# Optimization experiments

Measured on AMD Instinct MI355X. Metric: run time of the kernel, lower is better.

Reference implementation:

```python
import jax, jax.numpy as jnp
import numpy as np

B, L, D_PAIR, N_HEAD = 1, 320, 128, 4
EPS = 1e-5


def setup_inputs() -> dict:
    key = jax.random.key(0)
    ks = jax.random.split(key, 8)
    s = 0.05  # ~xavier scale for fan_in=128
    return {
        "pair": jax.random.normal(ks[0], (B, L, L, D_PAIR), jnp.float32),
        "norm_w": jnp.ones((D_PAIR,), jnp.float32),
        "norm_b": jnp.zeros((D_PAIR,), jnp.float32),
        "Wq": jax.random.normal(ks[1], (D_PAIR, D_PAIR), jnp.float32) * s,
        "Wk": jax.random.normal(ks[2], (D_PAIR, D_PAIR), jnp.float32) * s,
        "Wv": jax.random.normal(ks[3], (D_PAIR, D_PAIR), jnp.float32) * s,
        "Wg": jax.random.normal(ks[4], (D_PAIR, D_PAIR), jnp.float32) * s,
        "bg": jnp.zeros((D_PAIR,), jnp.float32),
        "Wo": jax.random.normal(ks[5], (D_PAIR, D_PAIR), jnp.float32) * s,
        "bo": jnp.zeros((D_PAIR,), jnp.float32),
        "Wb": jax.random.normal(ks[6], (N_HEAD, D_PAIR), jnp.float32) * s,
    }


def reference(pair, norm_w, norm_b, Wq, Wk, Wv, Wg, bg, Wo, bo, Wb):
    # Triangle attention, mode='start' (no permute). pair: (B, L, L, D)
    Bs, Ls, _, D = pair.shape
    H = Wb.shape[0]
    Dh = D // H
    scale = Dh ** -0.5

    # LayerNorm (fp32, matches torch eps=1e-5)
    mu = jnp.mean(pair, axis=-1, keepdims=True)
    var = jnp.var(pair, axis=-1, keepdims=True)
    x = (pair - mu) * jax.lax.rsqrt(var + EPS) * norm_w + norm_b

    def heads(y):
        # (B,L,L,D) -> (B,L,H,L,Dh): attention runs along the second L axis per row i
        return y.reshape(Bs, Ls, Ls, H, Dh).transpose(0, 1, 3, 2, 4)

    Q = heads(x @ Wq.T)
    K = heads(x @ Wk.T)
    V = heads(x @ Wv.T)
    g = heads(jax.nn.sigmoid(x @ Wg.T + bg))

    attn = jnp.einsum('blhid,blhjd->blhij', Q, K) * scale  # (B,L,H,L,L)
    # bias from RAW pair (pre-norm), projected to heads, broadcast over query index i
    bias = (pair @ Wb.T).transpose(0, 1, 3, 2)[:, :, :, None, :]  # (B,L,H,1,L)
    attn = jax.nn.softmax(attn + bias, axis=-1)

    out = jnp.einsum('blhij,blhjd->blhid', attn, V)  # (B,L,H,L,Dh)
    out = (g * out).transpose(0, 1, 3, 2, 4).reshape(Bs, Ls, Ls, D)
    return pair + out @ Wo.T + bo
```

## Files before the change

### kernel.cpp

```cpp
#include <hip/hip_runtime.h>

typedef unsigned short u16;
typedef unsigned int u32;
typedef __attribute__((ext_vector_type(8))) short bf16x8;
typedef __attribute__((ext_vector_type(4))) float f32x4;
typedef __attribute__((ext_vector_type(2))) unsigned int u32x2;

#define LOG2E 1.4426950408889634f

__device__ __forceinline__ u16 f2bf(float f) {
    u32 u = __float_as_uint(f);
    u += 0x7fffu + ((u >> 16) & 1u);
    return (u16)(u >> 16);
}
__device__ __forceinline__ float bf2f(u16 s) {
    return __uint_as_float(((u32)s) << 16);
}
__device__ __forceinline__ u32 pk_bf_trunc(float hi, float lo) {
    return __builtin_amdgcn_perm(__float_as_uint(hi), __float_as_uint(lo), 0x07060302u);
}

__global__ void wconv_kernel(const float* __restrict__ Wq, const float* __restrict__ Wk,
                             const float* __restrict__ Wv, const float* __restrict__ Wg,
                             const float* __restrict__ Wo, u16* __restrict__ wbf) {
    int idx = blockIdx.x * blockDim.x + threadIdx.x;
    wbf[0 * 16384 + idx] = f2bf(Wq[idx]);
    wbf[1 * 16384 + idx] = f2bf(Wk[idx]);
    wbf[2 * 16384 + idx] = f2bf(Wv[idx]);
    wbf[3 * 16384 + idx] = f2bf(Wg[idx]);
    wbf[4 * 16384 + idx] = f2bf(Wo[idx]);
}

#define PBUF_W 2688
#define QS_OFF 21504
#define KS_OFF 34304
#define GS_OFF 47104
#define VTS_OFF 59904

__global__ __launch_bounds__(512, 2)
void attn_kernel(const float* __restrict__ pair,
                 const float* __restrict__ norm_w,
                 const float* __restrict__ norm_b,
                 const float* __restrict__ bg,
                 const float* __restrict__ Wb,
                 const u16* __restrict__ wbf,
                 u16* __restrict__ Obf) {
    const int l = blockIdx.x >> 2;
    const int h = blockIdx.x & 3;
    const int tid = threadIdx.x;
    const int wave = tid >> 6;
    const int lane = tid & 63;
    const int i_lo = lane & 15;
    const int q = lane >> 4;

    __shared__ __align__(16) u16 smem[70400];
    __shared__ __align__(16) float biasLds[320];
    __shared__ __align__(16) float wls[3 * 128];

    if (tid < 96) {
        int a = tid >> 5;
        int t = tid & 31;
        const float* src = (a == 0) ? norm_w : (a == 1) ? norm_b : (Wb + h * 128);
        f32x4 v = *(const f32x4*)(src + t * 4);
        *(f32x4*)&wls[a * 128 + t * 4] = v;
    }

    float bg0 = bg[h * 32 + i_lo];
    float bg1 = bg[h * 32 + 16 + i_lo];

    bf16x8 wfrag[4][8];
#pragma unroll
    for (int kc = 0; kc < 4; ++kc)
#pragma unroll
        for (int nt = 0; nt < 8; ++nt) {
            int mat = nt >> 1;
            int drow = h * 32 + (nt & 1) * 16 + i_lo;
            wfrag[kc][nt] = *(const bf16x8*)&wbf[mat * 16384 + drow * 128 + kc * 32 + q * 8];
        }

    __syncthreads();

    const int row_g = tid >> 2;
    const int c4 = tid & 3;

#pragma unroll 1
    for (int t = 0; t < 3; ++t) {
        const int j0 = t * 128;
        const int nrows = (t == 2) ? 64 : 128;
        const bool act = row_g < nrows;

        f32x4 pr[8];
        float mu, rs, bd;
        if (act) {
            const float* prow = pair + ((size_t)(l * 320 + j0 + row_g)) * 128 + c4 * 32;
#pragma unroll
            for (int u = 0; u < 8; ++u) pr[u] = *(const f32x4*)(prow + u * 4);
            float s = 0.f, s2 = 0.f;
            bd = 0.f;
#pragma unroll
            for (int u = 0; u < 8; ++u) {
                f32x4 p = pr[u];
                f32x4 wb4 = *(const f32x4*)&wls[2 * 128 + c4 * 32 + u * 4];
                s += p[0] + p[1] + p[2] + p[3];
                s2 += p[0] * p[0] + p[1] * p[1] + p[2] * p[2] + p[3] * p[3];
                bd += p[0] * wb4[0] + p[1] * wb4[1] + p[2] * wb4[2] + p[3] * wb4[3];
            }
            s += __shfl_xor(s, 1);   s += __shfl_xor(s, 2);
            s2 += __shfl_xor(s2, 1); s2 += __shfl_xor(s2, 2);
            bd += __shfl_xor(bd, 1); bd += __shfl_xor(bd, 2);
            mu = s * 0.0078125f;
            float var = s2 * 0.0078125f - mu * mu;
            rs = rsqrtf(var + 1e-5f);
        }

        __syncthreads();
        if (act) {
#pragma unroll
            for (int u = 0; u < 8; ++u) {
                f32x4 p = pr[u];
                f32x4 w4 = *(const f32x4*)&wls[0 * 128 + c4 * 32 + u * 4];
                f32x4 b4 = *(const f32x4*)&wls[1 * 128 + c4 * 32 + u * 4];
                ushort4 xv;
                xv.x = f2bf((p[0] - mu) * rs * w4[0] + b4[0]);
                xv.y = f2bf((p[1] - mu) * rs * w4[1] + b4[1]);
                xv.z = f2bf((p[2] - mu) * rs * w4[2] + b4[2]);
                xv.w = f2bf((p[3] - mu) * rs * w4[3] + b4[3]);
                *(ushort4*)&smem[row_g * 136 + c4 * 32 + u * 4] = xv;
            }
            if (c4 == 0) biasLds[j0 + row_g] = bd * LOG2E;
        }
        __syncthreads();

        if (wave * 16 < nrows) {
            f32x4 acc[8];
#pragma unroll
            for (int nt = 0; nt < 8; ++nt) acc[nt] = (f32x4){0.f, 0.f, 0.f, 0.f};
#pragma unroll
            for (int kc = 0; kc < 4; ++kc) {
                bf16x8 a = *(const bf16x8*)&smem[(wave * 16 + i_lo) * 136 + kc * 32 + q * 8];
#pragma unroll
                for (int nt = 0; nt < 8; ++nt)
                    acc[nt] = __builtin_amdgcn_mfma_f32_16x16x32_bf16(a, wfrag[kc][nt], acc[nt], 0, 0, 0);
            }
            int jrow = j0 + wave * 16 + q * 4;
#pragma unroll
            for (int nt = 0; nt < 8; ++nt) {
#pragma unroll
                for (int r = 0; r < 4; ++r) {
                    float v = acc[nt][r];
                    int jr = jrow + r;
                    int dl = (nt & 1) * 16 + i_lo;
                    if (nt < 2)      smem[QS_OFF + jr * 40 + dl] = f2bf(v);
                    else if (nt < 4) smem[KS_OFF + jr * 40 + dl] = f2bf(v);
                    else if (nt < 6) smem[VTS_OFF + dl * 328 + jr] = f2bf(v);
                    else {
                        float z = v + ((nt & 1) ? bg1 : bg0);
                        float g = 1.0f / (1.0f + exp2f(-z * LOG2E));
                        smem[GS_OFF + jr * 40 + dl] = f2bf(g);
                    }
                }
            }
        }
    }
    __syncthreads();

    const float SC = 0.17677669529663687f * LOG2E;
    const f32x4 zero4 = {0.f, 0.f, 0.f, 0.f};
    u16* pb = smem + wave * PBUF_W;
#pragma unroll 1
    for (int t2 = 0; t2 < 3; ++t2) {
        const int strip = wave + 8 * t2;
        if (strip >= 20) break;
        const int i0 = strip * 16;
        bf16x8 qf = *(const bf16x8*)&smem[QS_OFF + (i0 + i_lo) * 40 + q * 8];

        f32x4 sc[20];
#pragma unroll
        for (int jt = 0; jt < 20; ++jt) {
            bf16x8 kf = *(const bf16x8*)&smem[KS_OFF + (jt * 16 + i_lo) * 40 + q * 8];
            sc[jt] = __builtin_amdgcn_mfma_f32_16x16x32_bf16(kf, qf, zero4, 0, 0, 0);
        }
        float sum = 0.f;
#pragma unroll
        for (int jt = 0; jt < 20; ++jt) {
            f32x4 b4 = *(const f32x4*)&biasLds[jt * 16 + q * 4];
#pragma unroll
            for (int r = 0; r < 4; ++r) {
                float p = exp2f(sc[jt][r] * SC + b4[r]);
                sc[jt][r] = p;
                sum += p;
            }
        }
        sum += __shfl_xor(sum, 16);
        sum += __shfl_xor(sum, 32);
        float rinv = 1.0f / sum;

        f32x4 oacc[2];
        oacc[0] = zero4; oacc[1] = zero4;
#pragma unroll
        for (int hh = 0; hh < 2; ++hh) {
#pragma unroll
            for (int jt10 = 0; jt10 < 10; ++jt10) {
                f32x4 s4 = sc[hh * 10 + jt10];
                u32x2 pk;
                pk.x = pk_bf_trunc(s4[1], s4[0]);
                pk.y = pk_bf_trunc(s4[3], s4[2]);
                *(u32x2*)&pb[i_lo * 168 + jt10 * 16 + q * 4] = pk;
            }
#pragma unroll
            for (int kt = 0; kt < 5; ++kt) {
                bf16x8 pf = *(const bf16x8*)&pb[i_lo * 168 + kt * 32 + q * 8];
#pragma unroll
                for (int mt = 0; mt < 2; ++mt) {
                    bf16x8 vf = *(const bf16x8*)&smem[VTS_OFF + (mt * 16 + i_lo) * 328 + hh * 160 + kt * 32 + q * 8];
                    oacc[mt] = __builtin_amdgcn_mfma_f32_16x16x32_bf16(vf, pf, oacc[mt], 0, 0, 0);
                }
            }
        }
#pragma unroll
        for (int mt = 0; mt < 2; ++mt) {
            ushort4 g4 = *(const ushort4*)&smem[GS_OFF + (i0 + i_lo) * 40 + mt * 16 + q * 4];
            float o0 = oacc[mt][0] * rinv * bf2f(g4.x);
            float o1 = oacc[mt][1] * rinv * bf2f(g4.y);
            float o2 = oacc[mt][2] * rinv * bf2f(g4.z);
            float o3 = oacc[mt][3] * rinv * bf2f(g4.w);
            u32x2 pk;
            pk.x = pk_bf_trunc(o1, o0);
            pk.y = pk_bf_trunc(o3, o2);
            *(u32x2*)&Obf[((size_t)(l * 320 + i0 + i_lo)) * 128 + h * 32 + mt * 16 + q * 4] = pk;
        }
    }
}

__global__ __launch_bounds__(256)
void outproj_kernel(const float* __restrict__ pair,
                    const float* __restrict__ bo,
                    const u16* __restrict__ Obf,
                    const u16* __restrict__ wbf,
                    float* __restrict__ out) {
    const int tid = threadIdx.x;
    const int wave = tid >> 6;
    const int lane = tid & 63;
    const int i_lo = lane & 15;
    const int q = lane >> 4;
    const int mrow = blockIdx.x * 64 + wave * 16;
    const u16* Wo = wbf + 4 * 16384;

    bf16x8 of[4];
#pragma unroll
    for (int kc = 0; kc < 4; ++kc)
        of[kc] = *(const bf16x8*)&Obf[((size_t)(mrow + i_lo)) * 128 + kc * 32 + q * 8];

    f32x4 acc[8];
#pragma unroll
    for (int nt = 0; nt < 8; ++nt) acc[nt] = (f32x4){0.f, 0.f, 0.f, 0.f};
#pragma unroll
    for (int nt = 0; nt < 8; ++nt) {
#pragma unroll
        for (int kc = 0; kc < 4; ++kc) {
            bf16x8 wf = *(const bf16x8*)&Wo[(nt * 16 + i_lo) * 128 + kc * 32 + q * 8];
            acc[nt] = __builtin_amdgcn_mfma_f32_16x16x32_bf16(wf, of[kc], acc[nt], 0, 0, 0);
        }
    }
#pragma unroll
    for (int nt = 0; nt < 8; ++nt) {
        size_t idx = ((size_t)(mrow + i_lo)) * 128 + nt * 16 + q * 4;
        f32x4 p4 = *(const f32x4*)&pair[idx];
        f32x4 b4 = *(const f32x4*)&bo[nt * 16 + q * 4];
        f32x4 o4;
        o4[0] = acc[nt][0] + p4[0] + b4[0];
        o4[1] = acc[nt][1] + p4[1] + b4[1];
        o4[2] = acc[nt][2] + p4[2] + b4[2];
        o4[3] = acc[nt][3] + p4[3] + b4[3];
        *(f32x4*)&out[idx] = o4;
    }
}

extern "C" void kernel_launch(void* const* d_in, const int* in_sizes, int n_in,
                              void* d_out, int out_size, void* d_ws, size_t ws_size,
                              hipStream_t stream) {
    const float* pair   = (const float*)d_in[0];
    const float* norm_w = (const float*)d_in[1];
    const float* norm_b = (const float*)d_in[2];
    const float* Wq     = (const float*)d_in[3];
    const float* Wk     = (const float*)d_in[4];
    const float* Wv     = (const float*)d_in[5];
    const float* Wg     = (const float*)d_in[6];
    const float* bg     = (const float*)d_in[7];
    const float* Wo     = (const float*)d_in[8];
    const float* bo     = (const float*)d_in[9];
    const float* Wb     = (const float*)d_in[10];

    u16* wbf = (u16*)d_ws;
    u16* Obf = wbf + 5 * 16384;
    float* out = (float*)d_out;

    wconv_kernel<<<64, 256, 0, stream>>>(Wq, Wk, Wv, Wg, Wo, wbf);
    attn_kernel<<<320 * 4, 512, 0, stream>>>(pair, norm_w, norm_b, bg, Wb, wbf, Obf);
    outproj_kernel<<<1600, 256, 0, stream>>>(pair, bo, Obf, wbf, out);
}
```

Measured before the change: 291.0 us.

## Shrink attention LDS and registers to raise occupancy; move gating into outproj

Cuts shared memory from about 140KB to about 65KB and raises launch bounds to 4 blocks per CU. To get there, Q is kept in registers instead of LDS, the gate is written to a global buffer and applied in the output-projection kernel, and projection weights are loaded from global memory per tile instead of held in registers. The projection now runs over 64-row tiles, with the Q/K and V/G column halves split across wave groups. Softmax and PV are processed in 64-column chunks so fewer score registers are live. The trade-off is extra global traffic for the gate buffer, repeated weight loads and more barriers, plus a second bf16 rounding of the gated output.

```diff
diff --git a/kernel.cpp b/kernel.cpp
--- a/kernel.cpp
+++ b/kernel.cpp
@@ -31,20 +31,19 @@
     wbf[4 * 16384 + idx] = f2bf(Wo[idx]);
 }
 
-#define PBUF_W 2688
-#define QS_OFF 21504
-#define KS_OFF 34304
-#define GS_OFF 47104
-#define VTS_OFF 59904
-
-__global__ __launch_bounds__(512, 2)
+#define KS_OFF 9216
+#define VTS_OFF 22016
+#define PB_W 1152
+
+__global__ __launch_bounds__(512, 4)
 void attn_kernel(const float* __restrict__ pair,
                  const float* __restrict__ norm_w,
                  const float* __restrict__ norm_b,
                  const float* __restrict__ bg,
                  const float* __restrict__ Wb,
                  const u16* __restrict__ wbf,
-                 u16* __restrict__ Obf) {
+                 u16* __restrict__ Obf,
+                 u16* __restrict__ Gg) {
     const int l = blockIdx.x >> 2;
     const int h = blockIdx.x & 3;
     const int tid = threadIdx.x;
@@ -53,9 +52,9 @@
     const int i_lo = lane & 15;
     const int q = lane >> 4;
 
-    __shared__ __align__(16) u16 smem[70400];
+    __shared__ __align__(16) u16 smem[32512];
     __shared__ __align__(16) float biasLds[320];
-    __shared__ __align__(16) float wls[3 * 128];
+    __shared__ __align__(16) float wls[384];
 
     if (tid < 96) {
         int a = tid >> 5;
@@ -68,165 +67,166 @@
     float bg0 = bg[h * 32 + i_lo];
     float bg1 = bg[h * 32 + 16 + i_lo];
 
-    bf16x8 wfrag[4][8];
-#pragma unroll
-    for (int kc = 0; kc < 4; ++kc)
-#pragma unroll
-        for (int nt = 0; nt < 8; ++nt) {
-            int mat = nt >> 1;
-            int drow = h * 32 + (nt & 1) * 16 + i_lo;
-            wfrag[kc][nt] = *(const bf16x8*)&wbf[mat * 16384 + drow * 128 + kc * 32 + q * 8];
-        }
-
     __syncthreads();
 
-    const int row_g = tid >> 2;
-    const int c4 = tid & 3;
+    const int row_g = tid >> 3;
+    const int c8 = tid & 7;
+    const int wrow = (wave & 3) * 16;
+    const int nth_flip = wave >> 2;
+
+    u32 qkeep[3][4];
 
 #pragma unroll 1
-    for (int t = 0; t < 3; ++t) {
-        const int j0 = t * 128;
-        const int nrows = (t == 2) ? 64 : 128;
-        const bool act = row_g < nrows;
-
-        f32x4 pr[8];
-        float mu, rs, bd;
-        if (act) {
-            const float* prow = pair + ((size_t)(l * 320 + j0 + row_g)) * 128 + c4 * 32;
-#pragma unroll
-            for (int u = 0; u < 8; ++u) pr[u] = *(const f32x4*)(prow + u * 4);
-            float s = 0.f, s2 = 0.f;
-            bd = 0.f;
-#pragma unroll
-            for (int u = 0; u < 8; ++u) {
-                f32x4 p = pr[u];
-                f32x4 wb4 = *(const f32x4*)&wls[2 * 128 + c4 * 32 + u * 4];
-                s += p[0] + p[1] + p[2] + p[3];
-                s2 += p[0] * p[0] + p[1] * p[1] + p[2] * p[2] + p[3] * p[3];
-                bd += p[0] * wb4[0] + p[1] * wb4[1] + p[2] * wb4[2] + p[3] * wb4[3];
-            }
-            s += __shfl_xor(s, 1);   s += __shfl_xor(s, 2);
-            s2 += __shfl_xor(s2, 1); s2 += __shfl_xor(s2, 2);
-            bd += __shfl_xor(bd, 1); bd += __shfl_xor(bd, 2);
-            mu = s * 0.0078125f;
-            float var = s2 * 0.0078125f - mu * mu;
-            rs = rsqrtf(var + 1e-5f);
-        }
+    for (int t = 0; t < 5; ++t) {
+        const int j0 = t * 64;
+        const float* prow = pair + ((size_t)(l * 320 + j0 + row_g)) * 128 + c8 * 16;
+        f32x4 pr[4];
+#pragma unroll
+        for (int u = 0; u < 4; ++u) pr[u] = *(const f32x4*)(prow + u * 4);
+
+        float s = 0.f, s2 = 0.f, bd = 0.f;
+#pragma unroll
+        for (int u = 0; u < 4; ++u) {
+            f32x4 p = pr[u];
+            f32x4 wb4 = *(const f32x4*)&wls[256 + c8 * 16 + u * 4];
+            s += p[0] + p[1] + p[2] + p[3];
+            s2 += p[0] * p[0] + p[1] * p[1] + p[2] * p[2] + p[3] * p[3];
+            bd += p[0] * wb4[0] + p[1] * wb4[1] + p[2] * wb4[2] + p[3] * wb4[3];
+        }
+        s += __shfl_xor(s, 1);   s += __shfl_xor(s, 2);   s += __shfl_xor(s, 4);
+        s2 += __shfl_xor(s2, 1); s2 += __shfl_xor(s2, 2); s2 += __shfl_xor(s2, 4);
+        bd += __shfl_xor(bd, 1); bd += __shfl_xor(bd, 2); bd += __shfl_xor(bd, 4);
+        float mu = s * 0.0078125f;
+        float var = s2 * 0.0078125f - mu * mu;
+        float rs = rsqrtf(var + 1e-5f);
 
         __syncthreads();
-        if (act) {
-#pragma unroll
-            for (int u = 0; u < 8; ++u) {
-                f32x4 p = pr[u];
-                f32x4 w4 = *(const f32x4*)&wls[0 * 128 + c4 * 32 + u * 4];
-                f32x4 b4 = *(const f32x4*)&wls[1 * 128 + c4 * 32 + u * 4];
-                ushort4 xv;
-                xv.x = f2bf((p[0] - mu) * rs * w4[0] + b4[0]);
-                xv.y = f2bf((p[1] - mu) * rs * w4[1] + b4[1]);
-                xv.z = f2bf((p[2] - mu) * rs * w4[2] + b4[2]);
-                xv.w = f2bf((p[3] - mu) * rs * w4[3] + b4[3]);
-                *(ushort4*)&smem[row_g * 136 + c4 * 32 + u * 4] = xv;
-            }
-            if (c4 == 0) biasLds[j0 + row_g] = bd * LOG2E;
-        }
+#pragma unroll
+        for (int u = 0; u < 4; ++u) {
+            f32x4 p = pr[u];
+            f32x4 w4 = *(const f32x4*)&wls[0 + c8 * 16 + u * 4];
+            f32x4 b4 = *(const f32x4*)&wls[128 + c8 * 16 + u * 4];
+            ushort4 xv;
+            xv.x = f2bf((p[0] - mu) * rs * w4[0] + b4[0]);
+            xv.y = f2bf((p[1] - mu) * rs * w4[1] + b4[1]);
+            xv.z = f2bf((p[2] - mu) * rs * w4[2] + b4[2]);
+            xv.w = f2bf((p[3] - mu) * rs * w4[3] + b4[3]);
+            *(ushort4*)&smem[row_g * 136 + c8 * 16 + u * 4] = xv;
+        }
+        if (c8 == 0) biasLds[j0 + row_g] = bd * LOG2E;
         __syncthreads();
 
-        if (wave * 16 < nrows) {
-            f32x4 acc[8];
-#pragma unroll
-            for (int nt = 0; nt < 8; ++nt) acc[nt] = (f32x4){0.f, 0.f, 0.f, 0.f};
-#pragma unroll
-            for (int kc = 0; kc < 4; ++kc) {
-                bf16x8 a = *(const bf16x8*)&smem[(wave * 16 + i_lo) * 136 + kc * 32 + q * 8];
-#pragma unroll
-                for (int nt = 0; nt < 8; ++nt)
-                    acc[nt] = __builtin_amdgcn_mfma_f32_16x16x32_bf16(a, wfrag[kc][nt], acc[nt], 0, 0, 0);
-            }
-            int jrow = j0 + wave * 16 + q * 4;
-#pragma unroll
-            for (int nt = 0; nt < 8; ++nt) {
+        const int nth = (t & 1) ^ nth_flip;
+        f32x4 acc[4];
+#pragma unroll
+        for (int n2 = 0; n2 < 4; ++n2) acc[n2] = (f32x4){0.f, 0.f, 0.f, 0.f};
+#pragma unroll
+        for (int kc = 0; kc < 4; ++kc) {
+            bf16x8 a = *(const bf16x8*)&smem[(wrow + i_lo) * 136 + kc * 32 + q * 8];
+#pragma unroll
+            for (int n2 = 0; n2 < 4; ++n2) {
+                int nt = nth * 4 + n2;
+                bf16x8 wf = *(const bf16x8*)&wbf[(nt >> 1) * 16384 +
+                                                 (h * 32 + (nt & 1) * 16 + i_lo) * 128 + kc * 32 + q * 8];
+                acc[n2] = __builtin_amdgcn_mfma_f32_16x16x32_bf16(a, wf, acc[n2], 0, 0, 0);
+            }
+        }
+        const int jrow = j0 + wrow + q * 4;
+        if (nth == 0) {
+            const int ti = t >> 1;
+#pragma unroll
+            for (int dd = 0; dd < 2; ++dd)
+#pragma unroll
+                for (int rr = 0; rr < 2; ++rr)
+                    qkeep[ti][dd * 2 + rr] =
+                        (u32)f2bf(acc[dd][rr * 2]) | ((u32)f2bf(acc[dd][rr * 2 + 1]) << 16);
+#pragma unroll
+            for (int n2 = 2; n2 < 4; ++n2)
+#pragma unroll
+                for (int r = 0; r < 4; ++r)
+                    smem[KS_OFF + (jrow + r) * 40 + (n2 & 1) * 16 + i_lo] = f2bf(acc[n2][r]);
+        } else {
+#pragma unroll
+            for (int n2 = 0; n2 < 2; ++n2)
+#pragma unroll
+                for (int r = 0; r < 4; ++r)
+                    smem[VTS_OFF + (n2 * 16 + i_lo) * 328 + jrow + r] = f2bf(acc[n2][r]);
+#pragma unroll
+            for (int n2 = 2; n2 < 4; ++n2)
 #pragma unroll
                 for (int r = 0; r < 4; ++r) {
-                    float v = acc[nt][r];
-                    int jr = jrow + r;
-                    int dl = (nt & 1) * 16 + i_lo;
-                    if (nt < 2)      smem[QS_OFF + jr * 40 + dl] = f2bf(v);
-                    else if (nt < 4) smem[KS_OFF + jr * 40 + dl] = f2bf(v);
-                    else if (nt < 6) smem[VTS_OFF + dl * 328 + jr] = f2bf(v);
-                    else {
-                        float z = v + ((nt & 1) ? bg1 : bg0);
-                        float g = 1.0f / (1.0f + exp2f(-z * LOG2E));
-                        smem[GS_OFF + jr * 40 + dl] = f2bf(g);
-                    }
+                    float z = acc[n2][r] + ((n2 & 1) ? bg1 : bg0);
+                    float g = 1.0f / (1.0f + exp2f(-z * LOG2E));
+                    Gg[((size_t)((l * 4 + h) * 320 + jrow + r)) * 32 + (n2 & 1) * 16 + i_lo] = f2bf(g);
                 }
-            }
         }
     }
     __syncthreads();
 
     const float SC = 0.17677669529663687f * LOG2E;
     const f32x4 zero4 = {0.f, 0.f, 0.f, 0.f};
-    u16* pb = smem + wave * PBUF_W;
+    u16* pb = smem + wave * PB_W;
+    const int nstrip = (wave < 4) ? 3 : 2;
 #pragma unroll 1
-    for (int t2 = 0; t2 < 3; ++t2) {
-        const int strip = wave + 8 * t2;
-        if (strip >= 20) break;
-        const int i0 = strip * 16;
-        bf16x8 qf = *(const bf16x8*)&smem[QS_OFF + (i0 + i_lo) * 40 + q * 8];
-
-        f32x4 sc[20];
-#pragma unroll
-        for (int jt = 0; jt < 20; ++jt) {
-            bf16x8 kf = *(const bf16x8*)&smem[KS_OFF + (jt * 16 + i_lo) * 40 + q * 8];
-            sc[jt] = __builtin_amdgcn_mfma_f32_16x16x32_bf16(kf, qf, zero4, 0, 0, 0);
-        }
+    for (int t2 = 0; t2 < nstrip; ++t2) {
+        const int i0 = (wave + 8 * t2) * 16;
+#pragma unroll
+        for (int dd = 0; dd < 2; ++dd)
+#pragma unroll
+            for (int rr = 0; rr < 2; ++rr) {
+                u32 v = qkeep[t2][dd * 2 + rr];
+                pb[(q * 4 + rr * 2) * 40 + dd * 16 + i_lo] = (u16)v;
+                pb[(q * 4 + rr * 2 + 1) * 40 + dd * 16 + i_lo] = (u16)(v >> 16);
+            }
+        bf16x8 qf = *(const bf16x8*)&pb[i_lo * 40 + q * 8];
+
+        f32x4 oacc[2];
+        oacc[0] = zero4; oacc[1] = zero4;
         float sum = 0.f;
-#pragma unroll
-        for (int jt = 0; jt < 20; ++jt) {
-            f32x4 b4 = *(const f32x4*)&biasLds[jt * 16 + q * 4];
-#pragma unroll
-            for (int r = 0; r < 4; ++r) {
-                float p = exp2f(sc[jt][r] * SC + b4[r]);
-                sc[jt][r] = p;
-                sum += p;
+#pragma unroll 1
+        for (int c = 0; c < 5; ++c) {
+            f32x4 sc4[4];
+#pragma unroll
+            for (int jt = 0; jt < 4; ++jt) {
+                bf16x8 kf = *(const bf16x8*)&smem[KS_OFF + (c * 64 + jt * 16 + i_lo) * 40 + q * 8];
+                sc4[jt] = __builtin_amdgcn_mfma_f32_16x16x32_bf16(kf, qf, zero4, 0, 0, 0);
+            }
+#pragma unroll
+            for (int jt = 0; jt < 4; ++jt) {
+                f32x4 b4 = *(const f32x4*)&biasLds[c * 64 + jt * 16 + q * 4];
+#pragma unroll
+                for (int r = 0; r < 4; ++r) {
+                    float p = exp2f(sc4[jt][r] * SC + b4[r]);
+                    sc4[jt][r] = p;
+                    sum += p;
+                }
+            }
+#pragma unroll
+            for (int jt = 0; jt < 4; ++jt) {
+                u32x2 pk;
+                pk.x = pk_bf_trunc(sc4[jt][1], sc4[jt][0]);
+                pk.y = pk_bf_trunc(sc4[jt][3], sc4[jt][2]);
+                *(u32x2*)&pb[i_lo * 72 + jt * 16 + q * 4] = pk;
+            }
+#pragma unroll
+            for (int kt2 = 0; kt2 < 2; ++kt2) {
+                bf16x8 pf = *(const bf16x8*)&pb[i_lo * 72 + kt2 * 32 + q * 8];
+#pragma unroll
+                for (int mt = 0; mt < 2; ++mt) {
+                    bf16x8 vf = *(const bf16x8*)&smem[VTS_OFF + (mt * 16 + i_lo) * 328 +
+                                                      c * 64 + kt2 * 32 + q * 8];
+                    oacc[mt] = __builtin_amdgcn_mfma_f32_16x16x32_bf16(vf, pf, oacc[mt], 0, 0, 0);
+                }
             }
         }
         sum += __shfl_xor(sum, 16);
         sum += __shfl_xor(sum, 32);
         float rinv = 1.0f / sum;
-
-        f32x4 oacc[2];
-        oacc[0] = zero4; oacc[1] = zero4;
-#pragma unroll
-        for (int hh = 0; hh < 2; ++hh) {
-#pragma unroll
-            for (int jt10 = 0; jt10 < 10; ++jt10) {
-                f32x4 s4 = sc[hh * 10 + jt10];
-                u32x2 pk;
-                pk.x = pk_bf_trunc(s4[1], s4[0]);
-                pk.y = pk_bf_trunc(s4[3], s4[2]);
-                *(u32x2*)&pb[i_lo * 168 + jt10 * 16 + q * 4] = pk;
-            }
-#pragma unroll
-            for (int kt = 0; kt < 5; ++kt) {
-                bf16x8 pf = *(const bf16x8*)&pb[i_lo * 168 + kt * 32 + q * 8];
-#pragma unroll
-                for (int mt = 0; mt < 2; ++mt) {
-                    bf16x8 vf = *(const bf16x8*)&smem[VTS_OFF + (mt * 16 + i_lo) * 328 + hh * 160 + kt * 32 + q * 8];
-                    oacc[mt] = __builtin_amdgcn_mfma_f32_16x16x32_bf16(vf, pf, oacc[mt], 0, 0, 0);
-                }
-            }
-        }
 #pragma unroll
         for (int mt = 0; mt < 2; ++mt) {
-            ushort4 g4 = *(const ushort4*)&smem[GS_OFF + (i0 + i_lo) * 40 + mt * 16 + q * 4];
-            float o0 = oacc[mt][0] * rinv * bf2f(g4.x);
-            float o1 = oacc[mt][1] * rinv * bf2f(g4.y);
-            float o2 = oacc[mt][2] * rinv * bf2f(g4.z);
-            float o3 = oacc[mt][3] * rinv * bf2f(g4.w);
             u32x2 pk;
-            pk.x = pk_bf_trunc(o1, o0);
-            pk.y = pk_bf_trunc(o3, o2);
+            pk.x = pk_bf_trunc(oacc[mt][1] * rinv, oacc[mt][0] * rinv);
+            pk.y = pk_bf_trunc(oacc[mt][3] * rinv, oacc[mt][2] * rinv);
             *(u32x2*)&Obf[((size_t)(l * 320 + i0 + i_lo)) * 128 + h * 32 + mt * 16 + q * 4] = pk;
         }
     }
@@ -236,6 +236,7 @@
 void outproj_kernel(const float* __restrict__ pair,
                     const float* __restrict__ bo,
                     const u16* __restrict__ Obf,
+                    const u16* __restrict__ Gg,
                     const u16* __restrict__ wbf,
                     float* __restrict__ out) {
     const int tid = threadIdx.x;
@@ -243,13 +244,26 @@
     const int lane = tid & 63;
     const int i_lo = lane & 15;
     const int q = lane >> 4;
-    const int mrow = blockIdx.x * 64 + wave * 16;
+    const int blk = blockIdx.x;
+    const int mrow = blk * 64 + wave * 16;
+    const int lidx = blk / 5;
+    const int irow = mrow - lidx * 320 + i_lo;
     const u16* Wo = wbf + 4 * 16384;
 
     bf16x8 of[4];
 #pragma unroll
-    for (int kc = 0; kc < 4; ++kc)
-        of[kc] = *(const bf16x8*)&Obf[((size_t)(mrow + i_lo)) * 128 + kc * 32 + q * 8];
+    for (int kc = 0; kc < 4; ++kc) {
+        union { bf16x8 v; u32 u[4]; } A, G, R;
+        A.v = *(const bf16x8*)&Obf[((size_t)(mrow + i_lo)) * 128 + kc * 32 + q * 8];
+        G.v = *(const bf16x8*)&Gg[((size_t)((lidx * 4 + kc) * 320 + irow)) * 32 + q * 8];
+#pragma unroll
+        for (int k4 = 0; k4 < 4; ++k4) {
+            float lo = __uint_as_float(A.u[k4] << 16) * __uint_as_float(G.u[k4] << 16);
+            float hi = __uint_as_float(A.u[k4] & 0xffff0000u) * __uint_as_float(G.u[k4] & 0xffff0000u);
+            R.u[k4] = pk_bf_trunc(hi, lo);
+        }
+        of[kc] = R.v;
+    }
 
     f32x4 acc[8];
 #pragma unroll
@@ -293,9 +307,10 @@
 
     u16* wbf = (u16*)d_ws;
     u16* Obf = wbf + 5 * 16384;
+    u16* Gg  = Obf + (size_t)102400 * 128;
     float* out = (float*)d_out;
 
     wconv_kernel<<<64, 256, 0, stream>>>(Wq, Wk, Wv, Wg, Wo, wbf);
-    attn_kernel<<<320 * 4, 512, 0, stream>>>(pair, norm_w, norm_b, bg, Wb, wbf, Obf);
-    outproj_kernel<<<1600, 256, 0, stream>>>(pair, bo, Obf, wbf, out);
-}
+    attn_kernel<<<320 * 4, 512, 0, stream>>>(pair, norm_w, norm_b, bg, Wb, wbf, Obf, Gg);
+    outproj_kernel<<<1600, 256, 0, stream>>>(pair, bo, Obf, Gg, wbf, out);
+}
```

Result: no change. 294.5 us (+1.2%).
